# Performance work log

Hardware: AMD Instinct MI355X
Metric: run time of the kernel (lower is better)

Reference implementation:

```python
import jax, jax.numpy as jnp
import numpy as np

K_RBF = 50
RBF_MU = jnp.asarray(np.linspace(0.0, 5.0, K_RBF), dtype=jnp.float32)
RBF_GAMMA = 10.0


def _lin(x, W, b=None):
    y = x @ W
    return y if b is None else y + b


def setup_inputs() -> dict:
    key = jax.random.key(0)
    B, N, F, H, C, K = 1, 512, 64, 64, 32, K_RBF

    def lin_p(k, fin, fout, bias=True):
        k1, k2 = jax.random.split(k)
        lim = float(1.0 / np.sqrt(fin))
        W = jax.random.uniform(k1, (fin, fout), minval=-lim, maxval=lim, dtype=jnp.float32)
        if not bias:
            return (W,)
        b = jax.random.uniform(k2, (fout,), minval=-lim, maxval=lim, dtype=jnp.float32)
        return (W, b)

    ks = jax.random.split(key, 13)
    h = jax.random.normal(ks[0], (B, N, F), dtype=jnp.float32)
    x = jax.random.normal(ks[1], (B, N, 3), dtype=jnp.float32)
    W_df_in, b_df_in = lin_p(ks[2], 2 * F, K)
    W_df1, b_df1 = lin_p(ks[3], K, H)
    W_df2, b_df2 = lin_p(ks[4], H, H)
    W_ew, b_ew = lin_p(ks[5], 2 * F + H, C)
    W_pn1, b_pn1 = lin_p(ks[6], C, H)
    W_pn2, b_pn2 = lin_p(ks[7], H, H)
    W_nm1, b_nm1 = lin_p(ks[8], 2 * H + F, H)
    W_nm2, b_nm2 = lin_p(ks[9], H, H)
    W_cm1, b_cm1 = lin_p(ks[10], H, H)
    W_cm2, b_cm2 = lin_p(ks[11], H, 1)
    (W_sa,) = lin_p(ks[12], 2 * F, 1, bias=False)
    return dict(h=h, x=x,
                W_df_in=W_df_in, b_df_in=b_df_in, W_df1=W_df1, b_df1=b_df1,
                W_df2=W_df2, b_df2=b_df2, W_ew=W_ew, b_ew=b_ew,
                W_pn1=W_pn1, b_pn1=b_pn1, W_pn2=W_pn2, b_pn2=b_pn2,
                W_nm1=W_nm1, b_nm1=b_nm1, W_nm2=W_nm2, b_nm2=b_nm2,
                W_cm1=W_cm1, b_cm1=b_cm1, W_cm2=W_cm2, b_cm2=b_cm2, W_sa=W_sa)


def reference(h, x, W_df_in, b_df_in, W_df1, b_df1, W_df2, b_df2,
              W_ew, b_ew, W_pn1, b_pn1, W_pn2, b_pn2,
              W_nm1, b_nm1, W_nm2, b_nm2,
              W_cm1, b_cm1, W_cm2, b_cm2, W_sa):
    B, N, F = h.shape
    # pairwise displacement: x_minus_xt[b,i,j] = x[b,j] - x[b,i]  -> [B,N,N,3]
    x_minus_xt = x[:, None, :, :] - x[:, :, None, :]
    d2 = jnp.sum(x_minus_xt ** 2, axis=-1, keepdims=True)          # [B,N,N,1]
    dist = jnp.sqrt(jnp.maximum(d2, 0.0) + 1e-14)                  # [B,N,N,1]
    spatial_att = jax.nn.softmax(dist, axis=-2)                    # softmax over j

    # h_cat_ht[b,i,j] = [h[b,j], h[b,i]]  -> [B,N,N,2F]
    h_j = jnp.broadcast_to(h[:, None, :, :], (B, N, N, F))
    h_i = jnp.broadcast_to(h[:, :, None, :], (B, N, N, F))
    h_cat_ht = jnp.concatenate([h_j, h_i], axis=-1)

    # continuous filter convolution: rbf(dist) gated projection + 2-layer MLP
    rbf = jnp.exp(-RBF_GAMMA * (dist - RBF_MU) ** 2)               # [B,N,N,K]
    he = _lin(h_cat_ht, W_df_in, b_df_in) * rbf
    he = _lin(jax.nn.silu(_lin(he, W_df1, b_df1)), W_df2, b_df2)   # [B,N,N,H]

    semantic_att = jax.nn.softmax(jax.nn.silu(_lin(h_cat_ht, W_sa)), axis=-2)  # [B,N,N,1]

    w_edge = jnp.tanh(_lin(jnp.concatenate([h_cat_ht, he], axis=-1), W_ew, b_ew))  # [B,N,N,C]
    x_dir = x_minus_xt / (d2 + 1e-5)                               # [B,N,N,3]
    x_att = w_edge[..., None] * x_dir[..., None, :]                # [B,N,N,C,3]
    x_att_sum = jnp.sum(x_att, axis=-3)                            # sum over j -> [B,N,C,3]
    x_att_norm = jnp.sqrt(jnp.maximum(jnp.sum(x_att_sum ** 2, -1), 0.0) + 1e-14)  # [B,N,C]
    norm_emb = _lin(jax.nn.silu(_lin(x_att_norm, W_pn1, b_pn1)), W_pn2, b_pn2)    # [B,N,H]

    coord_w = _lin(jax.nn.silu(_lin(he, W_cm1, b_cm1)), W_cm2, b_cm2)  # [B,N,N,1]
    x_new = jnp.sum(x_minus_xt * coord_w, axis=-2) + x                 # [B,N,3]

    total_att = jax.nn.softmax(semantic_att * spatial_att, axis=-2)    # [B,N,N,1]
    he_agg = jnp.sum(total_att * he, axis=-2)                          # [B,N,H]

    node_in = jnp.concatenate([h, he_agg, norm_emb], axis=-1)          # [B,N,F+2H]
    h_new = _lin(jax.nn.silu(_lin(node_in, W_nm1, b_nm1)), W_nm2, b_nm2)
    return h_new, x_new
```

## Files before the change

### kernel.cpp

```cpp
#include <hip/hip_runtime.h>
#include <math.h>

#define NN 512
#define FF 64
#define HH 64
#define CC 32
#define KK 50

typedef unsigned int uint;
typedef short bhalf8_t __attribute__((ext_vector_type(8)));
typedef float f32x4_t __attribute__((ext_vector_type(4)));
#define MFMA16 __builtin_amdgcn_mfma_f32_16x16x32_bf16

union FragA { bhalf8_t v; uint u[4]; short4 h[2]; };

__device__ __forceinline__ float frcp(float x){ return __builtin_amdgcn_rcpf(x); }
__device__ __forceinline__ float fsilu(float x){ return x * frcp(1.0f + __expf(-x)); }
__device__ __forceinline__ float ftanh(float x){ return 1.0f - 2.0f * frcp(__expf(2.0f*x) + 1.0f); }
__device__ __forceinline__ short f2bf(float f){
    uint u = __float_as_uint(f);
    return (short)((u + 0x7FFFu + ((u >> 16) & 1u)) >> 16);
}
__device__ __forceinline__ uint pack2(float lo, float hi){
    return (uint)(unsigned short)f2bf(lo) | ((uint)(unsigned short)f2bf(hi) << 16);
}

__device__ __forceinline__ float bfly_max(float v){
    #pragma unroll
    for (int m = 1; m < 64; m <<= 1) v = fmaxf(v, __shfl_xor(v, m, 64));
    return v;
}
__device__ __forceinline__ float bfly_sum(float v){
    #pragma unroll
    for (int m = 1; m < 64; m <<= 1) v += __shfl_xor(v, m, 64);
    return v;
}
__device__ __forceinline__ float block_max8(float v, float* red, int lane, int wid){
    v = bfly_max(v);
    __syncthreads();
    if (lane == 0) red[wid] = v;
    __syncthreads();
    float m = red[0];
    #pragma unroll
    for (int k = 1; k < 8; ++k) m = fmaxf(m, red[k]);
    return m;
}
__device__ __forceinline__ float block_sum8(float v, float* red, int lane, int wid){
    v = bfly_sum(v);
    __syncthreads();
    if (lane == 0) red[wid] = v;
    __syncthreads();
    float s = red[0];
    #pragma unroll
    for (int k = 1; k < 8; ++k) s += red[k];
    return s;
}

extern "C" __global__ __launch_bounds__(128)
void sake_pre(const float* __restrict__ h,
              const float* __restrict__ W_df_in, const float* __restrict__ b_df_in,
              const float* __restrict__ W_ew,    const float* __restrict__ b_ew,
              const float* __restrict__ W_sa,
              const float* __restrict__ W_df1, const float* __restrict__ W_df2,
              const float* __restrict__ W_cm1,
              float* __restrict__ Am, float* __restrict__ Cm,
              float* __restrict__ Em, float* __restrict__ Fm,
              float* __restrict__ sa, float* __restrict__ sb,
              short* __restrict__ Wf1, short* __restrict__ Wf2,
              short* __restrict__ Wfc, short* __restrict__ Wfe)
{
    const int b = blockIdx.x;
    const int t = threadIdx.x;
    if (b < NN) {
        __shared__ float hrow[FF];
        if (t < FF) hrow[t] = h[b*FF + t];
        __syncthreads();
        if (t < 64) {
            if (t < KK) {
                float a_ = 0.f, c_ = b_df_in[t];
                #pragma unroll 8
                for (int f = 0; f < FF; ++f) {
                    a_ += hrow[f] * W_df_in[f*KK + t];
                    c_ += hrow[f] * W_df_in[(FF+f)*KK + t];
                }
                Am[b*64 + t] = a_;
                Cm[b*64 + t] = c_;
            } else {
                Am[b*64 + t] = 0.f;
                Cm[b*64 + t] = 0.f;
            }
        } else if (t < 96) {
            int cc = t - 64;
            float e = 0.f, ff2 = b_ew[cc];
            #pragma unroll 8
            for (int f = 0; f < FF; ++f) {
                e   += hrow[f] * W_ew[f*CC + cc];
                ff2 += hrow[f] * W_ew[(FF+f)*CC + cc];
            }
            Em[b*CC + cc] = e;
            Fm[b*CC + cc] = ff2;
        } else if (t == 96) {
            float v = 0.f;
            #pragma unroll 8
            for (int f = 0; f < FF; ++f) v += hrow[f] * W_sa[f];
            sa[b] = v;
        } else if (t == 97) {
            float v = 0.f;
            #pragma unroll 8
            for (int f = 0; f < FF; ++f) v += hrow[f] * W_sa[FF + f];
            sb[b] = v;
        }
    } else {
        const int wb = b - NN;
        const int cnt = (wb == 3) ? 2048 : 4096;
        for (int idx = t; idx < cnt; idx += 128) {
            int q  = idx & 7;
            int l  = (idx >> 3) & 63;
            int ks = (idx >> 9) & 1;
            int nt = idx >> 10;
            int k  = 32*ks + 8*(l >> 4) + q;
            int n  = 16*nt + (l & 15);
            float v;
            if (wb == 0)      v = (k < KK) ? W_df1[k*HH + n] : 0.f;
            else if (wb == 1) v = W_df2[k*HH + n];
            else if (wb == 2) v = W_cm1[k*HH + n];
            else              v = W_ew[(128 + k)*CC + n];
            short* dst = (wb == 0) ? Wf1 : (wb == 1) ? Wf2 : (wb == 2) ? Wfc : Wfe;
            dst[idx] = f2bf(v);
        }
    }
}

#define OFF_W1   0
#define OFF_W2   8192
#define OFF_WC   16384
#define OFF_WE   24576
#define OFF_TILE 28672
#define OFF_DIST 48128
#define OFF_DX   50176
#define OFF_ATTW 56320
#define OFF_CORD 58368
#define OFF_SCM  60416
#define OFF_SB1  60672
#define OFF_SB2  60928
#define OFF_SBC1 61184
#define OFF_WC2  61440
#define OFF_FM   61696
#define OFF_BC2  61824
#define SMEM_BYTES 61952

extern "C" __global__ __launch_bounds__(512)
void sake_main(const float* __restrict__ x,
               const float* __restrict__ b_df1, const float* __restrict__ b_df2,
               const float* __restrict__ b_cm1,
               const float* __restrict__ W_cm2, const float* __restrict__ b_cm2,
               const float* __restrict__ Am, const float* __restrict__ Cm,
               const float* __restrict__ Em, const float* __restrict__ Fm,
               const float* __restrict__ sa, const float* __restrict__ sb,
               const short* __restrict__ Wf1, const short* __restrict__ Wf2,
               const short* __restrict__ Wfc, const short* __restrict__ Wfe,
               float* __restrict__ heagg, float* __restrict__ xan,
               float* __restrict__ out)
{
    extern __shared__ char smem[];
    short* sW1    = (short*)(smem + OFF_W1);
    short* sW2    = (short*)(smem + OFF_W2);
    short* sWc    = (short*)(smem + OFF_WC);
    short* sWe    = (short*)(smem + OFF_WE);
    float* dist_s = (float*)(smem + OFF_DIST);
    float* dx_s   = (float*)(smem + OFF_DX);
    float* attw_s = (float*)(smem + OFF_ATTW);
    float* cord_s = (float*)(smem + OFF_CORD);
    float* sCm    = (float*)(smem + OFF_SCM);
    float* sB1    = (float*)(smem + OFF_SB1);
    float* sB2    = (float*)(smem + OFF_SB2);
    float* sBc1   = (float*)(smem + OFF_SBC1);
    float* sWc2   = (float*)(smem + OFF_WC2);
    float* sFm    = (float*)(smem + OFF_FM);
    float* sBc2   = (float*)(smem + OFF_BC2);

    __shared__ float red[8];
    __shared__ float sAggH[8][64];
    __shared__ float sAccX[8][96];
    __shared__ float xatt_f[96];

    const int i   = blockIdx.x;
    const int tid = threadIdx.x;

    ((uint4*)sW1)[tid] = ((const uint4*)Wf1)[tid];
    ((uint4*)sW2)[tid] = ((const uint4*)Wf2)[tid];
    ((uint4*)sWc)[tid] = ((const uint4*)Wfc)[tid];
    if (tid < 256) ((uint4*)sWe)[tid] = ((const uint4*)Wfe)[tid];
    if (tid < 64) {
        sCm[tid]  = Cm[i*64 + tid];
        sB1[tid]  = b_df1[tid];
        sB2[tid]  = b_df2[tid];
        sBc1[tid] = b_cm1[tid];
        sWc2[tid] = W_cm2[tid];
    }
    if (tid < 32) sFm[tid] = Fm[i*CC + tid];
    if (tid == 0) sBc2[0] = b_cm2[0];

    const float xi0 = x[i*3+0], xi1 = x[i*3+1], xi2 = x[i*3+2];
    const float sbi = sb[i];
    const int lane = tid & 63, wid = tid >> 6;
    {
        const int j = tid;
        float d0 = x[j*3+0]-xi0, d1 = x[j*3+1]-xi1, d2c = x[j*3+2]-xi2;
        float d2 = d0*d0 + d1*d1 + d2c*d2c;
        float dj = sqrtf(d2 + 1e-14f);
        float sv = fsilu(sa[j] + sbi);
        dist_s[j] = dj;
        dx_s[j*3+0] = d0; dx_s[j*3+1] = d1; dx_s[j*3+2] = d2c;
        float dmax = block_max8(dj, red, lane, wid);
        float dsum = block_sum8(__expf(dj - dmax), red, lane, wid);
        float smax = block_max8(sv, red, lane, wid);
        float ssum = block_sum8(__expf(sv - smax), red, lane, wid);
        float p = __expf((dj - dmax) + (sv - smax)) * frcp(dsum * ssum);
        float pmax = block_max8(p, red, lane, wid);
        float te = __expf(p - pmax);
        float tsum = block_sum8(te, red, lane, wid);
        attw_s[j] = te * frcp(tsum);
    }
    __syncthreads();

    const int w = wid, l = lane, a = l & 15, g = l >> 4;
    const float gf = (float)(8 * g);
    short* myTile = (short*)(smem + OFF_TILE) + w * (16 * 76);
    const float4* Amv  = (const float4*)Am;
    const float4* sCmv = (const float4*)sCm;

    float b1n[4], b2n[4], bcn[4], wc2r[4];
    #pragma unroll
    for (int nt = 0; nt < 4; ++nt) {
        b1n[nt]  = sB1[16*nt + a];
        b2n[nt]  = sB2[16*nt + a];
        bcn[nt]  = sBc1[16*nt + a];
        wc2r[nt] = sWc2[16*nt + a];
    }
    float fmr0 = sFm[a], fmr1 = sFm[16 + a];
    const float bc2v = sBc2[0];

    float aggH[4] = {0.f, 0.f, 0.f, 0.f};
    float xAcc[6] = {0.f, 0.f, 0.f, 0.f, 0.f, 0.f};

    const float MUK  = 5.0f / 49.0f;
    const float RBFC = -14.4269504f;

    #pragma unroll 1
    for (int t = 0; t < 4; ++t) {
        const int Mb   = w*64 + t*16;
        const int jrow = Mb + a;
        const int jred = Mb + 4*g;
        const float dj = dist_s[jrow];

        FragA a0, a1;
        #pragma unroll
        for (int s = 0; s < 2; ++s) {
            float4 amL = Amv[jrow*16 + s*8 + g*2];
            float4 amH = Amv[jrow*16 + s*8 + g*2 + 1];
            float4 cmL = sCmv[s*8 + g*2];
            float4 cmH = sCmv[s*8 + g*2 + 1];
            float vq[8];
            vq[0] = amL.x + cmL.x; vq[1] = amL.y + cmL.y;
            vq[2] = amL.z + cmL.z; vq[3] = amL.w + cmL.w;
            vq[4] = amH.x + cmH.x; vq[5] = amH.y + cmH.y;
            vq[6] = amH.z + cmH.z; vq[7] = amH.w + cmH.w;
            #pragma unroll
            for (int q = 0; q < 8; ++q) {
                float kf = gf + (float)(32*s + q);
                float dd = dj - kf * MUK;
                vq[q] *= exp2f(dd * dd * RBFC);
            }
            FragA* ap = s ? &a1 : &a0;
            ap->u[0] = pack2(vq[0], vq[1]);
            ap->u[1] = pack2(vq[2], vq[3]);
            ap->u[2] = pack2(vq[4], vq[5]);
            ap->u[3] = pack2(vq[6], vq[7]);
        }

        f32x4_t acc[4];
        #pragma unroll
        for (int nt = 0; nt < 4; ++nt) acc[nt] = (f32x4_t){b1n[nt], b1n[nt], b1n[nt], b1n[nt]};
        #pragma unroll
        for (int s = 0; s < 2; ++s) {
            bhalf8_t av = s ? a1.v : a0.v;
            #pragma unroll
            for (int nt = 0; nt < 4; ++nt) {
                bhalf8_t bv = *(const bhalf8_t*)&sW1[((nt*2 + s)*64 + l)*8];
                acc[nt] = MFMA16(av, bv, acc[nt], 0, 0, 0);
            }
        }
        #pragma unroll
        for (int nt = 0; nt < 4; ++nt) {
            #pragma unroll
            for (int r = 0; r < 4; ++r)
                myTile[(4*g + r)*76 + a + 16*nt] = f2bf(fsilu(acc[nt][r]));
        }

        FragA h0, h1;
        h0.h[0] = *(const short4*)&myTile[a*76 + 8*g];
        h0.h[1] = *(const short4*)&myTile[a*76 + 8*g + 4];
        h1.h[0] = *(const short4*)&myTile[a*76 + 32 + 8*g];
        h1.h[1] = *(const short4*)&myTile[a*76 + 32 + 8*g + 4];
        #pragma unroll
        for (int nt = 0; nt < 4; ++nt) acc[nt] = (f32x4_t){b2n[nt], b2n[nt], b2n[nt], b2n[nt]};
        #pragma unroll
        for (int s = 0; s < 2; ++s) {
            bhalf8_t av = s ? h1.v : h0.v;
            #pragma unroll
            for (int nt = 0; nt < 4; ++nt) {
                bhalf8_t bv = *(const bhalf8_t*)&sW2[((nt*2 + s)*64 + l)*8];
                acc[nt] = MFMA16(av, bv, acc[nt], 0, 0, 0);
            }
        }
        float at0 = attw_s[jred+0], at1 = attw_s[jred+1],
              at2 = attw_s[jred+2], at3 = attw_s[jred+3];
        #pragma unroll
        for (int nt = 0; nt < 4; ++nt) {
            aggH[nt] += at0*acc[nt][0] + at1*acc[nt][1] + at2*acc[nt][2] + at3*acc[nt][3];
            #pragma unroll
            for (int r = 0; r < 4; ++r)
                myTile[(4*g + r)*76 + a + 16*nt] = f2bf(acc[nt][r]);
        }

        FragA e0, e1;
        e0.h[0] = *(const short4*)&myTile[a*76 + 8*g];
        e0.h[1] = *(const short4*)&myTile[a*76 + 8*g + 4];
        e1.h[0] = *(const short4*)&myTile[a*76 + 32 + 8*g];
        e1.h[1] = *(const short4*)&myTile[a*76 + 32 + 8*g + 4];

        f32x4_t ae[2];
        ae[0] = (f32x4_t){0.f,0.f,0.f,0.f};
        ae[1] = (f32x4_t){0.f,0.f,0.f,0.f};
        #pragma unroll
        for (int s = 0; s < 2; ++s) {
            bhalf8_t av = s ? e1.v : e0.v;
            #pragma unroll
            for (int nt = 0; nt < 2; ++nt) {
                bhalf8_t bv = *(const bhalf8_t*)&sWe[((nt*2 + s)*64 + l)*8];
                ae[nt] = MFMA16(av, bv, ae[nt], 0, 0, 0);
            }
        }
        float xd[4][3];
        #pragma unroll
        for (int r = 0; r < 4; ++r) {
            float dr = dist_s[jred + r];
            float iv = frcp(dr*dr + 1e-5f);
            xd[r][0] = dx_s[(jred+r)*3+0] * iv;
            xd[r][1] = dx_s[(jred+r)*3+1] * iv;
            xd[r][2] = dx_s[(jred+r)*3+2] * iv;
        }
        #pragma unroll
        for (int nt = 0; nt < 2; ++nt) {
            float fmv = nt ? fmr1 : fmr0;
            #pragma unroll
            for (int r = 0; r < 4; ++r) {
                float em = Em[(jred+r)*CC + a + 16*nt];
                float wv = ftanh(ae[nt][r] + em + fmv);
                xAcc[nt*3+0] += wv * xd[r][0];
                xAcc[nt*3+1] += wv * xd[r][1];
                xAcc[nt*3+2] += wv * xd[r][2];
            }
        }

        #pragma unroll
        for (int nt = 0; nt < 4; ++nt) acc[nt] = (f32x4_t){bcn[nt], bcn[nt], bcn[nt], bcn[nt]};
        #pragma unroll
        for (int s = 0; s < 2; ++s) {
            bhalf8_t av = s ? e1.v : e0.v;
            #pragma unroll
            for (int nt = 0; nt < 4; ++nt) {
                bhalf8_t bv = *(const bhalf8_t*)&sWc[((nt*2 + s)*64 + l)*8];
                acc[nt] = MFMA16(av, bv, acc[nt], 0, 0, 0);
            }
        }
        float cw[4] = {0.f, 0.f, 0.f, 0.f};
        #pragma unroll
        for (int nt = 0; nt < 4; ++nt) {
            #pragma unroll
            for (int r = 0; r < 4; ++r)
                cw[r] += fsilu(acc[nt][r]) * wc2r[nt];
        }
        #pragma unroll
        for (int m = 1; m < 16; m <<= 1) {
            #pragma unroll
            for (int r = 0; r < 4; ++r) cw[r] += __shfl_xor(cw[r], m, 64);
        }
        if (a == 0) {
            #pragma unroll
            for (int r = 0; r < 4; ++r) cord_s[jred + r] = cw[r] + bc2v;
        }
    }

    #pragma unroll
    for (int nt = 0; nt < 4; ++nt) {
        aggH[nt] += __shfl_xor(aggH[nt], 16, 64);
        aggH[nt] += __shfl_xor(aggH[nt], 32, 64);
    }
    #pragma unroll
    for (int q = 0; q < 6; ++q) {
        xAcc[q] += __shfl_xor(xAcc[q], 16, 64);
        xAcc[q] += __shfl_xor(xAcc[q], 32, 64);
    }
    if (l < 16) {
        #pragma unroll
        for (int nt = 0; nt < 4; ++nt) sAggH[w][l + 16*nt] = aggH[nt];
        #pragma unroll
        for (int d = 0; d < 3; ++d) {
            sAccX[w][l*3 + d]        = xAcc[d];
            sAccX[w][(l+16)*3 + d]   = xAcc[3 + d];
        }
    }
    __syncthreads();

    {
        float cwv = cord_s[tid];
        float X0 = block_sum8(dx_s[tid*3+0]*cwv, red, lane, wid);
        float X1 = block_sum8(dx_s[tid*3+1]*cwv, red, lane, wid);
        float X2 = block_sum8(dx_s[tid*3+2]*cwv, red, lane, wid);
        if (tid == 0) {
            out[NN*HH + i*3+0] = X0 + xi0;
            out[NN*HH + i*3+1] = X1 + xi1;
            out[NN*HH + i*3+2] = X2 + xi2;
        }
    }

    if (tid < 64) {
        float s = 0.f;
        #pragma unroll
        for (int ww = 0; ww < 8; ++ww) s += sAggH[ww][tid];
        heagg[i*64 + tid] = s;
    }
    if (tid < 96) {
        float s = 0.f;
        #pragma unroll
        for (int ww = 0; ww < 8; ++ww) s += sAccX[ww][tid];
        xatt_f[tid] = s;
    }
    __syncthreads();
    if (tid < 32) {
        float aa = xatt_f[tid*3+0], bb = xatt_f[tid*3+1], cc = xatt_f[tid*3+2];
        xan[i*32 + tid] = sqrtf(aa*aa + bb*bb + cc*cc + 1e-14f);
    }
}

extern "C" __global__ __launch_bounds__(64)
void sake_post(const float* __restrict__ h,
               const float* __restrict__ W_pn1, const float* __restrict__ b_pn1,
               const float* __restrict__ W_pn2, const float* __restrict__ b_pn2,
               const float* __restrict__ W_nm1, const float* __restrict__ b_nm1,
               const float* __restrict__ W_nm2, const float* __restrict__ b_nm2,
               const float* __restrict__ heagg, const float* __restrict__ xan,
               float* __restrict__ out)
{
    const int i = blockIdx.x;
    const int n = threadIdx.x;
    __shared__ float pn1_s[64];
    __shared__ float node_in[192];
    __shared__ float nm1_s[64];

    float acc = b_pn1[n];
    #pragma unroll
    for (int c = 0; c < CC; ++c) acc += xan[i*CC + c] * W_pn1[c*HH + n];
    pn1_s[n] = fsilu(acc);
    __syncthreads();

    acc = b_pn2[n];
    #pragma unroll 16
    for (int k = 0; k < HH; ++k) acc += pn1_s[k] * W_pn2[k*HH + n];
    node_in[128 + n] = acc;
    node_in[n]       = h[i*FF + n];
    node_in[64 + n]  = heagg[i*64 + n];
    __syncthreads();

    acc = b_nm1[n];
    #pragma unroll 16
    for (int k = 0; k < 192; ++k) acc += node_in[k] * W_nm1[k*HH + n];
    nm1_s[n] = fsilu(acc);
    __syncthreads();

    acc = b_nm2[n];
    #pragma unroll 16
    for (int k = 0; k < HH; ++k) acc += nm1_s[k] * W_nm2[k*HH + n];
    out[i*HH + n] = acc;
}

extern "C" void kernel_launch(void* const* d_in, const int* in_sizes, int n_in,
                              void* d_out, int out_size, void* d_ws, size_t ws_size,
                              hipStream_t stream)
{
    const float* h       = (const float*)d_in[0];
    const float* x       = (const float*)d_in[1];
    const float* W_df_in = (const float*)d_in[2];
    const float* b_df_in = (const float*)d_in[3];
    const float* W_df1   = (const float*)d_in[4];
    const float* b_df1   = (const float*)d_in[5];
    const float* W_df2   = (const float*)d_in[6];
    const float* b_df2   = (const float*)d_in[7];
    const float* W_ew    = (const float*)d_in[8];
    const float* b_ew    = (const float*)d_in[9];
    const float* W_pn1   = (const float*)d_in[10];
    const float* b_pn1   = (const float*)d_in[11];
    const float* W_pn2   = (const float*)d_in[12];
    const float* b_pn2   = (const float*)d_in[13];
    const float* W_nm1   = (const float*)d_in[14];
    const float* b_nm1   = (const float*)d_in[15];
    const float* W_nm2   = (const float*)d_in[16];
    const float* b_nm2   = (const float*)d_in[17];
    const float* W_cm1   = (const float*)d_in[18];
    const float* b_cm1   = (const float*)d_in[19];
    const float* W_cm2   = (const float*)d_in[20];
    const float* b_cm2   = (const float*)d_in[21];
    const float* W_sa    = (const float*)d_in[22];
    float* out = (float*)d_out;

    float* ws = (float*)d_ws;
    float* Am = ws;
    float* Cm = Am + 512*64;
    float* Em = Cm + 512*64;
    float* Fm = Em + 512*32;
    float* sa = Fm + 512*32;
    float* sb = sa + 512;
    short* Wf1 = (short*)(sb + 512);
    short* Wf2 = Wf1 + 4096;
    short* Wfc = Wf2 + 4096;
    short* Wfe = Wfc + 4096;
    float* heagg = (float*)(Wfe + 2048);
    float* xan   = heagg + 512*64;

    (void)hipFuncSetAttribute((const void*)sake_main,
        hipFuncAttributeMaxDynamicSharedMemorySize, SMEM_BYTES);

    sake_pre<<<NN + 4, 128, 0, stream>>>(h, W_df_in, b_df_in, W_ew, b_ew, W_sa,
                                         W_df1, W_df2, W_cm1,
                                         Am, Cm, Em, Fm, sa, sb,
                                         Wf1, Wf2, Wfc, Wfe);
    sake_main<<<NN, 512, SMEM_BYTES, stream>>>(x,
        b_df1, b_df2, b_cm1, W_cm2, b_cm2,
        Am, Cm, Em, Fm, sa, sb,
        Wf1, Wf2, Wfc, Wfe, heagg, xan, out);
    sake_post<<<NN, 64, 0, stream>>>(h,
        W_pn1, b_pn1, W_pn2, b_pn2, W_nm1, b_nm1, W_nm2, b_nm2,
        heagg, xan, out);
}
```

Measured before the change: 157.3 us.

## Halve main kernel block size and read MFMA weights from global instead of LDS

The main pair kernel now runs 256 threads (4 waves) per block, and each wave processes 8 row tiles instead of 4. The block reductions are resized to 4 waves, and each thread handles two j entries in the softmax prologue and the final coordinate sum. The bf16 weight fragments are no longer staged into shared memory. MFMA B operands are loaded straight from global (expected to hit in cache), which cuts LDS from about 62KB to about 23KB, allowing more resident blocks and removing the per-block staging copy. The trade-offs are repeated global or L2 loads in the inner MFMA loops and less intra-block parallelism.

```diff
diff --git a/kernel.cpp b/kernel.cpp
--- a/kernel.cpp
+++ b/kernel.cpp
@@ -35,25 +35,19 @@
     for (int m = 1; m < 64; m <<= 1) v += __shfl_xor(v, m, 64);
     return v;
 }
-__device__ __forceinline__ float block_max8(float v, float* red, int lane, int wid){
+__device__ __forceinline__ float block_max4(float v, float* red, int lane, int wid){
     v = bfly_max(v);
     __syncthreads();
     if (lane == 0) red[wid] = v;
     __syncthreads();
-    float m = red[0];
-    #pragma unroll
-    for (int k = 1; k < 8; ++k) m = fmaxf(m, red[k]);
-    return m;
-}
-__device__ __forceinline__ float block_sum8(float v, float* red, int lane, int wid){
+    return fmaxf(fmaxf(red[0], red[1]), fmaxf(red[2], red[3]));
+}
+__device__ __forceinline__ float block_sum4(float v, float* red, int lane, int wid){
     v = bfly_sum(v);
     __syncthreads();
     if (lane == 0) red[wid] = v;
     __syncthreads();
-    float s = red[0];
-    #pragma unroll
-    for (int k = 1; k < 8; ++k) s += red[k];
-    return s;
+    return (red[0] + red[1]) + (red[2] + red[3]);
 }
 
 extern "C" __global__ __launch_bounds__(128)
@@ -113,6 +107,7 @@
     } else {
         const int wb = b - NN;
         const int cnt = (wb == 3) ? 2048 : 4096;
+        #pragma unroll 4
         for (int idx = t; idx < cnt; idx += 128) {
             int q  = idx & 7;
             int l  = (idx >> 3) & 63;
@@ -131,25 +126,21 @@
     }
 }
 
-#define OFF_W1   0
-#define OFF_W2   8192
-#define OFF_WC   16384
-#define OFF_WE   24576
-#define OFF_TILE 28672
-#define OFF_DIST 48128
-#define OFF_DX   50176
-#define OFF_ATTW 56320
-#define OFF_CORD 58368
-#define OFF_SCM  60416
-#define OFF_SB1  60672
-#define OFF_SB2  60928
-#define OFF_SBC1 61184
-#define OFF_WC2  61440
-#define OFF_FM   61696
-#define OFF_BC2  61824
-#define SMEM_BYTES 61952
-
-extern "C" __global__ __launch_bounds__(512)
+#define OFF_TILE 0
+#define OFF_DIST 9728
+#define OFF_DX   11776
+#define OFF_ATTW 17920
+#define OFF_CORD 19968
+#define OFF_SCM  22016
+#define OFF_SB1  22272
+#define OFF_SB2  22528
+#define OFF_SBC1 22784
+#define OFF_WC2  23040
+#define OFF_FM   23296
+#define OFF_BC2  23424
+#define SMEM_BYTES 23552
+
+extern "C" __global__ __launch_bounds__(256)
 void sake_main(const float* __restrict__ x,
                const float* __restrict__ b_df1, const float* __restrict__ b_df2,
                const float* __restrict__ b_cm1,
@@ -163,10 +154,6 @@
                float* __restrict__ out)
 {
     extern __shared__ char smem[];
-    short* sW1    = (short*)(smem + OFF_W1);
-    short* sW2    = (short*)(smem + OFF_W2);
-    short* sWc    = (short*)(smem + OFF_WC);
-    short* sWe    = (short*)(smem + OFF_WE);
     float* dist_s = (float*)(smem + OFF_DIST);
     float* dx_s   = (float*)(smem + OFF_DX);
     float* attw_s = (float*)(smem + OFF_ATTW);
@@ -179,18 +166,15 @@
     float* sFm    = (float*)(smem + OFF_FM);
     float* sBc2   = (float*)(smem + OFF_BC2);
 
-    __shared__ float red[8];
-    __shared__ float sAggH[8][64];
-    __shared__ float sAccX[8][96];
+    __shared__ float red[4];
+    __shared__ float sAggH[4][64];
+    __shared__ float sAccX[4][96];
     __shared__ float xatt_f[96];
 
     const int i   = blockIdx.x;
     const int tid = threadIdx.x;
-
-    ((uint4*)sW1)[tid] = ((const uint4*)Wf1)[tid];
-    ((uint4*)sW2)[tid] = ((const uint4*)Wf2)[tid];
-    ((uint4*)sWc)[tid] = ((const uint4*)Wfc)[tid];
-    if (tid < 256) ((uint4*)sWe)[tid] = ((const uint4*)Wfe)[tid];
+    const int lane = tid & 63, wid = tid >> 6;
+
     if (tid < 64) {
         sCm[tid]  = Cm[i*64 + tid];
         sB1[tid]  = b_df1[tid];
@@ -203,24 +187,31 @@
 
     const float xi0 = x[i*3+0], xi1 = x[i*3+1], xi2 = x[i*3+2];
     const float sbi = sb[i];
-    const int lane = tid & 63, wid = tid >> 6;
     {
-        const int j = tid;
-        float d0 = x[j*3+0]-xi0, d1 = x[j*3+1]-xi1, d2c = x[j*3+2]-xi2;
-        float d2 = d0*d0 + d1*d1 + d2c*d2c;
-        float dj = sqrtf(d2 + 1e-14f);
-        float sv = fsilu(sa[j] + sbi);
-        dist_s[j] = dj;
-        dx_s[j*3+0] = d0; dx_s[j*3+1] = d1; dx_s[j*3+2] = d2c;
-        float dmax = block_max8(dj, red, lane, wid);
-        float dsum = block_sum8(__expf(dj - dmax), red, lane, wid);
-        float smax = block_max8(sv, red, lane, wid);
-        float ssum = block_sum8(__expf(sv - smax), red, lane, wid);
-        float p = __expf((dj - dmax) + (sv - smax)) * frcp(dsum * ssum);
-        float pmax = block_max8(p, red, lane, wid);
-        float te = __expf(p - pmax);
-        float tsum = block_sum8(te, red, lane, wid);
-        attw_s[j] = te * frcp(tsum);
+        float dj[2], sv[2];
+        #pragma unroll
+        for (int u = 0; u < 2; ++u) {
+            const int j = tid + u*256;
+            float d0 = x[j*3+0]-xi0, d1 = x[j*3+1]-xi1, d2c = x[j*3+2]-xi2;
+            float d2 = d0*d0 + d1*d1 + d2c*d2c;
+            dj[u] = sqrtf(d2 + 1e-14f);
+            sv[u] = fsilu(sa[j] + sbi);
+            dist_s[j] = dj[u];
+            dx_s[j*3+0] = d0; dx_s[j*3+1] = d1; dx_s[j*3+2] = d2c;
+        }
+        float dmax = block_max4(fmaxf(dj[0], dj[1]), red, lane, wid);
+        float dsum = block_sum4(__expf(dj[0]-dmax) + __expf(dj[1]-dmax), red, lane, wid);
+        float smax = block_max4(fmaxf(sv[0], sv[1]), red, lane, wid);
+        float ssum = block_sum4(__expf(sv[0]-smax) + __expf(sv[1]-smax), red, lane, wid);
+        float inv_ds = frcp(dsum * ssum);
+        float p0 = __expf((dj[0]-dmax) + (sv[0]-smax)) * inv_ds;
+        float p1 = __expf((dj[1]-dmax) + (sv[1]-smax)) * inv_ds;
+        float pmax = block_max4(fmaxf(p0, p1), red, lane, wid);
+        float t0 = __expf(p0 - pmax), t1 = __expf(p1 - pmax);
+        float tsum = block_sum4(t0 + t1, red, lane, wid);
+        float inv_tsum = frcp(tsum);
+        attw_s[tid]       = t0 * inv_tsum;
+        attw_s[tid + 256] = t1 * inv_tsum;
     }
     __syncthreads();
 
@@ -229,6 +220,10 @@
     short* myTile = (short*)(smem + OFF_TILE) + w * (16 * 76);
     const float4* Amv  = (const float4*)Am;
     const float4* sCmv = (const float4*)sCm;
+    const bhalf8_t* pW1 = (const bhalf8_t*)Wf1;
+    const bhalf8_t* pW2 = (const bhalf8_t*)Wf2;
+    const bhalf8_t* pWc = (const bhalf8_t*)Wfc;
+    const bhalf8_t* pWe = (const bhalf8_t*)Wfe;
 
     float b1n[4], b2n[4], bcn[4], wc2r[4];
     #pragma unroll
@@ -248,8 +243,8 @@
     const float RBFC = -14.4269504f;
 
     #pragma unroll 1
-    for (int t = 0; t < 4; ++t) {
-        const int Mb   = w*64 + t*16;
+    for (int t = 0; t < 8; ++t) {
+        const int Mb   = (w*8 + t)*16;
         const int jrow = Mb + a;
         const int jred = Mb + 4*g;
         const float dj = dist_s[jrow];
@@ -287,7 +282,7 @@
             bhalf8_t av = s ? a1.v : a0.v;
             #pragma unroll
             for (int nt = 0; nt < 4; ++nt) {
-                bhalf8_t bv = *(const bhalf8_t*)&sW1[((nt*2 + s)*64 + l)*8];
+                bhalf8_t bv = pW1[(nt*2 + s)*64 + l];
                 acc[nt] = MFMA16(av, bv, acc[nt], 0, 0, 0);
             }
         }
@@ -310,7 +305,7 @@
             bhalf8_t av = s ? h1.v : h0.v;
             #pragma unroll
             for (int nt = 0; nt < 4; ++nt) {
-                bhalf8_t bv = *(const bhalf8_t*)&sW2[((nt*2 + s)*64 + l)*8];
+                bhalf8_t bv = pW2[(nt*2 + s)*64 + l];
                 acc[nt] = MFMA16(av, bv, acc[nt], 0, 0, 0);
             }
         }
@@ -338,7 +333,7 @@
             bhalf8_t av = s ? e1.v : e0.v;
             #pragma unroll
             for (int nt = 0; nt < 2; ++nt) {
-                bhalf8_t bv = *(const bhalf8_t*)&sWe[((nt*2 + s)*64 + l)*8];
+                bhalf8_t bv = pWe[(nt*2 + s)*64 + l];
                 ae[nt] = MFMA16(av, bv, ae[nt], 0, 0, 0);
             }
         }
@@ -371,7 +366,7 @@
             bhalf8_t av = s ? e1.v : e0.v;
             #pragma unroll
             for (int nt = 0; nt < 4; ++nt) {
-                bhalf8_t bv = *(const bhalf8_t*)&sWc[((nt*2 + s)*64 + l)*8];
+                bhalf8_t bv = pWc[(nt*2 + s)*64 + l];
                 acc[nt] = MFMA16(av, bv, acc[nt], 0, 0, 0);
             }
         }
@@ -415,10 +410,10 @@
     __syncthreads();
 
     {
-        float cwv = cord_s[tid];
-        float X0 = block_sum8(dx_s[tid*3+0]*cwv, red, lane, wid);
-        float X1 = block_sum8(dx_s[tid*3+1]*cwv, red, lane, wid);
-        float X2 = block_sum8(dx_s[tid*3+2]*cwv, red, lane, wid);
+        float cw0 = cord_s[tid], cw1 = cord_s[tid + 256];
+        float X0 = block_sum4(dx_s[tid*3+0]*cw0 + dx_s[(tid+256)*3+0]*cw1, red, lane, wid);
+        float X1 = block_sum4(dx_s[tid*3+1]*cw0 + dx_s[(tid+256)*3+1]*cw1, red, lane, wid);
+        float X2 = block_sum4(dx_s[tid*3+2]*cw0 + dx_s[(tid+256)*3+2]*cw1, red, lane, wid);
         if (tid == 0) {
             out[NN*HH + i*3+0] = X0 + xi0;
             out[NN*HH + i*3+1] = X1 + xi1;
@@ -429,13 +424,13 @@
     if (tid < 64) {
         float s = 0.f;
         #pragma unroll
-        for (int ww = 0; ww < 8; ++ww) s += sAggH[ww][tid];
+        for (int ww = 0; ww < 4; ++ww) s += sAggH[ww][tid];
         heagg[i*64 + tid] = s;
     }
     if (tid < 96) {
         float s = 0.f;
         #pragma unroll
-        for (int ww = 0; ww < 8; ++ww) s += sAccX[ww][tid];
+        for (int ww = 0; ww < 4; ++ww) s += sAccX[ww][tid];
         xatt_f[tid] = s;
     }
     __syncthreads();
@@ -536,7 +531,7 @@
                                          W_df1, W_df2, W_cm1,
                                          Am, Cm, Em, Fm, sa, sb,
                                          Wf1, Wf2, Wfc, Wfe);
-    sake_main<<<NN, 512, SMEM_BYTES, stream>>>(x,
+    sake_main<<<NN, 256, SMEM_BYTES, stream>>>(x,
         b_df1, b_df2, b_cm1, W_cm2, b_cm2,
         Am, Cm, Em, Fm, sa, sb,
         Wf1, Wf2, Wfc, Wfe, heagg, xan, out);
```

Measured after the change: 162.7 us. +3.5%, slower.
